# Kernel tuning notes

Hardware: AMD Instinct MI355X
Metric: run time of the kernel (lower is better)

Reference implementation:

```python
import jax, jax.numpy as jnp
import numpy as np

N, E, H, C = 50000, 800000, 4, 32   # nodes, edges, heads, per-head channels
EMB = 64                              # embedding_dim
VOCAB = 1000                          # input_dim (label vocab)


def _gat_layer(x, src, dst, W, a_src, a_dst, b):
    """PyG GATConv (concat heads, negative_slope=0.2, self-loops already in src/dst)."""
    n = x.shape[0]
    h = (x @ W).reshape(n, H, -1)                 # [N,H,C]
    al_s = (h * a_src).sum(-1)                    # [N,H]
    al_d = (h * a_dst).sum(-1)                    # [N,H]
    e = jax.nn.leaky_relu(al_s[src] + al_d[dst], 0.2)   # [E',H]
    m = jax.ops.segment_max(e, dst, num_segments=n)     # segment softmax (stable)
    p = jnp.exp(e - m[dst])
    s = jax.ops.segment_sum(p, dst, num_segments=n)
    alpha = p / (s[dst] + 1e-16)                  # [E',H]
    out = jax.ops.segment_sum(h[src] * alpha[..., None], dst, num_segments=n)
    return out.reshape(n, -1) + b                 # [N,H*C]


def setup_inputs() -> dict:
    key = jax.random.key(0)
    ks = jax.random.split(key, 16)
    def w(k, shape):
        return jax.random.normal(k, shape, jnp.float32) * 0.1
    return dict(
        label=jax.random.randint(ks[0], (N,), 0, VOCAB),
        edge_index=jax.random.randint(ks[1], (2, E), 0, N),
        weight=jax.random.uniform(ks[2], (E,), jnp.float32),
        request_quantity=jax.random.uniform(ks[3], (N,), jnp.float32),
        emb_table=w(ks[4], (VOCAB, EMB)),
        req_W=w(ks[5], (1, EMB)),
        req_b=jnp.zeros((EMB,), jnp.float32),
        W0=w(ks[6], (2 * EMB, H * C)), a_src0=w(ks[7], (H, C)), a_dst0=w(ks[8], (H, C)), b0=jnp.zeros((H * C,), jnp.float32),
        W1=w(ks[9], (H * C, H * C)), a_src1=w(ks[10], (H, C)), a_dst1=w(ks[11], (H, C)), b1=jnp.zeros((H * C,), jnp.float32),
        W2=w(ks[12], (H * C, H * C)), a_src2=w(ks[13], (H, C)), a_dst2=w(ks[14], (H, C)), b2=jnp.zeros((H * C,), jnp.float32),
    )


def reference(label, edge_index, weight, request_quantity, emb_table, req_W, req_b,
              W0, a_src0, a_dst0, b0, W1, a_src1, a_dst1, b1, W2, a_src2, a_dst2, b2):
    del weight  # GATConv(edge_dim=None): edge weights are not used in attention
    x_emb = emb_table[label]                                  # [N,EMB]
    rq = request_quantity
    rq = (rq - rq.mean()) / (rq.std(ddof=1) + 1e-6)           # torch std uses ddof=1
    req = rq[:, None] @ req_W + req_b                         # [N,EMB]
    x = jnp.concatenate([x_emb, req], axis=-1)                # [N,2*EMB]
    # PyG GATConv adds self-loops by default
    loops = jnp.arange(N)
    src = jnp.concatenate([edge_index[0], loops])
    dst = jnp.concatenate([edge_index[1], loops])
    gelu = lambda t: jax.nn.gelu(t, approximate=False)        # torch nn.GELU is exact
    x = gelu(_gat_layer(x, src, dst, W0, a_src0, a_dst0, b0))
    x = gelu(_gat_layer(x, src, dst, W1, a_src1, a_dst1, b1))
    x = gelu(_gat_layer(x, src, dst, W2, a_src2, a_dst2, b2))
    return x
```

## Files before the change

### kernel.cpp

```cpp
#include <hip/hip_runtime.h>
#include <hip/hip_fp16.h>
#include <math.h>

#define NN 50000
#define NE 800000
#define HC 128
#define NHEAD 4
#define EMB 64
#define STATS_BLOCKS 64
#define NB 196
#define HIST_BLOCKS 196
#define WPREP_BLOCKS 192
#define WT_ROW 136

typedef _Float16 f16x8 __attribute__((ext_vector_type(8)));
typedef float f32x4 __attribute__((ext_vector_type(4)));

__device__ __forceinline__ float lrelu(float x) { return x > 0.0f ? x : 0.2f * x; }
__device__ __forceinline__ float gelu_f(float x) {
    return 0.5f * x * (1.0f + erff(x * 0.70710678118654752440f));
}
__device__ __forceinline__ float sel4(float4 v, int h) {
    float r = v.x;
    r = (h == 1) ? v.y : r;
    r = (h == 2) ? v.z : r;
    r = (h == 3) ? v.w : r;
    return r;
}
__device__ __forceinline__ f16x8 cvt8(float4 a, float4 b) {
    f16x8 v;
    v[0] = (_Float16)a.x; v[1] = (_Float16)a.y; v[2] = (_Float16)a.z; v[3] = (_Float16)a.w;
    v[4] = (_Float16)b.x; v[5] = (_Float16)b.y; v[6] = (_Float16)b.z; v[7] = (_Float16)b.w;
    return v;
}

__global__ void prep_kernel(const float* __restrict__ rq, float* __restrict__ stats,
                            const int* __restrict__ dst, int* __restrict__ bucketCnt,
                            const float* __restrict__ W0, const float* __restrict__ W1,
                            const float* __restrict__ W2, _Float16* __restrict__ wt) {
    __shared__ float ls[4], ls2[4];
    __shared__ int cnt[NB];
    if (blockIdx.x < STATS_BLOCKS) {
        int i = blockIdx.x * 256 + threadIdx.x;
        float s = 0.f, s2 = 0.f;
        for (; i < NN; i += STATS_BLOCKS * 256) {
            float v = rq[i];
            s += v; s2 += v * v;
        }
        #pragma unroll
        for (int off = 32; off > 0; off >>= 1) {
            s  += __shfl_down(s, off);
            s2 += __shfl_down(s2, off);
        }
        int lane = threadIdx.x & 63, wid = threadIdx.x >> 6;
        if (lane == 0) { ls[wid] = s; ls2[wid] = s2; }
        __syncthreads();
        if (threadIdx.x == 0) {
            atomicAdd(&stats[0], ls[0] + ls[1] + ls[2] + ls[3]);
            atomicAdd(&stats[1], ls2[0] + ls2[1] + ls2[2] + ls2[3]);
        }
    } else if (blockIdx.x < STATS_BLOCKS + HIST_BLOCKS) {
        int bb = blockIdx.x - STATS_BLOCKS;
        for (int i = threadIdx.x; i < NB; i += 256) cnt[i] = 0;
        __syncthreads();
        int base = bb * 4096;
        #pragma unroll
        for (int it = 0; it < 16; it++) {
            int i = base + it * 256 + threadIdx.x;
            if (i < NE) atomicAdd(&cnt[dst[i] >> 8], 1);
        }
        __syncthreads();
        for (int i = threadIdx.x; i < NB; i += 256)
            if (cnt[i]) atomicAdd(&bucketCnt[i], cnt[i]);
    } else {
        int bb = blockIdx.x - STATS_BLOCKS - HIST_BLOCKS;
        int l = bb >> 6, blk = bb & 63;
        const float* W = (l == 0) ? W0 : (l == 1) ? W1 : W2;
        int idx = blk * 256 + threadIdx.x;
        int n = idx >> 7, k = idx & 127;
        wt[(size_t)l * 128 * WT_ROW + n * WT_ROW + k] = (_Float16)W[k * 128 + n];
    }
}

__device__ __forceinline__ void scan_buckets(const int* __restrict__ bucketCnt,
                                             int* sIncl ) {
    int t = threadIdx.x;
    int v = (t < NB) ? bucketCnt[t] : 0;
    sIncl[t] = v;
    __syncthreads();
    #pragma unroll
    for (int off = 1; off < 256; off <<= 1) {
        int add = (t >= off) ? sIncl[t - off] : 0;
        __syncthreads();
        sIncl[t] += add;
        __syncthreads();
    }
}

__global__ void binA_kernel(const int* __restrict__ src, const int* __restrict__ dst,
                            const int* __restrict__ bucketCnt, int* __restrict__ gcur,
                            int2* __restrict__ edge_tmp) {
    __shared__ int sIncl[256];
    __shared__ int sBaseE[256];
    __shared__ int cnt[NB];
    __shared__ int cur[NB];
    int t = threadIdx.x;
    scan_buckets(bucketCnt, sIncl);
    {
        int v = (t < NB) ? bucketCnt[t] : 0;
        sBaseE[t] = sIncl[t] - v;
    }
    for (int i = t; i < NB; i += 256) cnt[i] = 0;
    __syncthreads();
    int base = blockIdx.x * 4096;
    int d[16], s[16];
    #pragma unroll
    for (int it = 0; it < 16; it++) {
        int i = base + it * 256 + t;
        bool ok = i < NE;
        d[it] = ok ? dst[i] : -1;
        s[it] = ok ? src[i] : 0;
        if (ok) atomicAdd(&cnt[d[it] >> 8], 1);
    }
    __syncthreads();
    for (int i = t; i < NB; i += 256)
        cur[i] = cnt[i] ? (sBaseE[i] + atomicAdd(&gcur[i], cnt[i])) : 0;
    __syncthreads();
    #pragma unroll
    for (int it = 0; it < 16; it++) {
        if (d[it] >= 0) {
            int b = d[it] >> 8;
            int pos = atomicAdd(&cur[b], 1);
            edge_tmp[pos] = make_int2(s[it], d[it] & 255);
        }
    }
}

__global__ void binB_kernel(const int2* __restrict__ edge_tmp, const int* __restrict__ bucketCnt,
                            int* __restrict__ row_start, int* __restrict__ src_sorted) {
    __shared__ int sIncl[256];
    __shared__ int ldeg[256];
    __shared__ int lexcl[256];
    __shared__ int lcur[256];
    __shared__ int s_base, s_end;
    int b = blockIdx.x, t = threadIdx.x;
    scan_buckets(bucketCnt, sIncl);
    if (t == 0) {
        s_end = sIncl[b];
        s_base = sIncl[b] - bucketCnt[b];
    }
    ldeg[t] = 0;
    __syncthreads();
    int base = s_base, endb = s_end;
    for (int i = base + t; i < endb; i += 256)
        atomicAdd(&ldeg[edge_tmp[i].y], 1);
    __syncthreads();
    int v = ldeg[t];
    lexcl[t] = v;
    __syncthreads();
    #pragma unroll
    for (int off = 1; off < 256; off <<= 1) {
        int add = (t >= off) ? lexcl[t - off] : 0;
        __syncthreads();
        lexcl[t] += add;
        __syncthreads();
    }
    int excl = lexcl[t] - v;
    int node = b * 256 + t;
    if (node <= NN) row_start[node] = base + excl;
    lcur[t] = excl;
    __syncthreads();
    for (int i = base + t; i < endb; i += 256) {
        int2 e = edge_tmp[i];
        int pos = atomicAdd(&lcur[e.y], 1);
        src_sorted[base + pos] = e.x;
    }
}

template <int L0>
__launch_bounds__(256)
__global__ void gemm_al_kernel(const __half* __restrict__ xh, const _Float16* __restrict__ wt,
                               const float* __restrict__ a_src, const float* __restrict__ a_dst,
                               __half* __restrict__ h, float* __restrict__ als,
                               float* __restrict__ ald,
                               const int* __restrict__ label, const float* __restrict__ rq,
                               const float* __restrict__ emb, const float* __restrict__ reqW,
                               const float* __restrict__ reqb, const float* __restrict__ stats) {
    extern __shared__ char smem[];
    _Float16* sWt = (_Float16*)smem;
    _Float16* sX  = sWt + 128 * WT_ROW;
    int t = threadIdx.x;
    int w = t >> 6, l = t & 63;
    int col = l & 15, quad = l >> 4;
    int row0 = blockIdx.x * 64;

    {
        const f16x8* g = (const f16x8*)wt;
        f16x8* s = (f16x8*)sWt;
        #pragma unroll
        for (int i = 0; i < 9; i++) {
            int idx = t + 256 * i;
            if (idx < 128 * WT_ROW / 8) s[idx] = g[idx];
        }
    }
    if (L0) {
        float sum = stats[0], sumsq = stats[1];
        float mean = sum / (float)NN;
        float var = (sumsq - sum * sum / (float)NN) / (float)(NN - 1);
        float inv = 1.0f / (sqrtf(var) + 1e-6f);
        #pragma unroll
        for (int i = 0; i < 4; i++) {
            int idx = t + 256 * i;
            int r = idx >> 4;
            int q = idx & 15;
            int rr = row0 + r;
            f16x8 v;
            #pragma unroll
            for (int j = 0; j < 8; j++) v[j] = (_Float16)0.f;
            if (rr < NN) {
                if (q < 8) {
                    const float4* er = (const float4*)(emb + (size_t)label[rr] * EMB);
                    v = cvt8(er[q * 2], er[q * 2 + 1]);
                } else {
                    int j4 = (q - 8) * 2;
                    float4 w0 = ((const float4*)reqW)[j4],     b0 = ((const float4*)reqb)[j4];
                    float4 w1 = ((const float4*)reqW)[j4 + 1], b1 = ((const float4*)reqb)[j4 + 1];
                    float r2 = (rq[rr] - mean) * inv;
                    v = cvt8(make_float4(r2 * w0.x + b0.x, r2 * w0.y + b0.y,
                                         r2 * w0.z + b0.z, r2 * w0.w + b0.w),
                             make_float4(r2 * w1.x + b1.x, r2 * w1.y + b1.y,
                                         r2 * w1.z + b1.z, r2 * w1.w + b1.w));
                }
            }
            *(f16x8*)&sX[r * WT_ROW + q * 8] = v;
        }
    }
    __syncthreads();

    f16x8 afr[4];
    if (L0) {
        #pragma unroll
        for (int ks = 0; ks < 4; ks++)
            afr[ks] = *(const f16x8*)&sX[(w * 16 + col) * WT_ROW + ks * 32 + quad * 8];
    } else {
        int rr = row0 + w * 16 + col;
        const __half* xp = xh + (size_t)rr * 128;
        #pragma unroll
        for (int ks = 0; ks < 4; ks++)
            afr[ks] = *(const f16x8*)(xp + ks * 32 + quad * 8);
    }

    f32x4 zero = {0.f, 0.f, 0.f, 0.f};
    f32x4 acc[8];
    #pragma unroll
    for (int nt = 0; nt < 8; nt++) acc[nt] = zero;
    #pragma unroll
    for (int nt = 0; nt < 8; nt++) {
        #pragma unroll
        for (int ks = 0; ks < 4; ks++) {
            f16x8 bfr = *(const f16x8*)&sWt[(nt * 16 + col) * WT_ROW + ks * 32 + quad * 8];
            acc[nt] = __builtin_amdgcn_mfma_f32_16x16x32_f16(afr[ks], bfr, acc[nt], 0, 0, 0);
        }
    }
    __syncthreads();

    _Float16* sOut = sWt;
    #pragma unroll
    for (int nt = 0; nt < 8; nt++)
        #pragma unroll
        for (int r = 0; r < 4; r++)
            sOut[(w * 16 + quad * 4 + r) * WT_ROW + nt * 16 + col] = (_Float16)acc[nt][r];
    __builtin_amdgcn_wave_barrier();
    #pragma unroll
    for (int i = 0; i < 4; i++) {
        int u = l + 64 * i;
        int r = u >> 4, off = (u & 15) * 8;
        int rr = row0 + w * 16 + r;
        f16x8 v = *(const f16x8*)&sOut[(w * 16 + r) * WT_ROW + off];
        if (rr < NN) *(f16x8*)(h + (size_t)rr * 128 + off) = v;
    }

    float as[8], ad[8];
    #pragma unroll
    for (int nt = 0; nt < 8; nt++) {
        as[nt] = a_src[nt * 16 + col];
        ad[nt] = a_dst[nt * 16 + col];
    }
    #pragma unroll
    for (int r = 0; r < 4; r++) {
        float ps[4], pd[4];
        #pragma unroll
        for (int hd = 0; hd < 4; hd++) {
            ps[hd] = acc[2 * hd][r] * as[2 * hd] + acc[2 * hd + 1][r] * as[2 * hd + 1];
            pd[hd] = acc[2 * hd][r] * ad[2 * hd] + acc[2 * hd + 1][r] * ad[2 * hd + 1];
            ps[hd] += __shfl_xor(ps[hd], 1); pd[hd] += __shfl_xor(pd[hd], 1);
            ps[hd] += __shfl_xor(ps[hd], 2); pd[hd] += __shfl_xor(pd[hd], 2);
            ps[hd] += __shfl_xor(ps[hd], 4); pd[hd] += __shfl_xor(pd[hd], 4);
            ps[hd] += __shfl_xor(ps[hd], 8); pd[hd] += __shfl_xor(pd[hd], 8);
        }
        int rr = row0 + w * 16 + quad * 4 + r;
        if (col == 0 && rr < NN) {
            *(float4*)(als + (size_t)rr * 4) = make_float4(ps[0], ps[1], ps[2], ps[3]);
            *(float4*)(ald + (size_t)rr * 4) = make_float4(pd[0], pd[1], pd[2], pd[3]);
        }
    }
}

template <int FINAL>
__launch_bounds__(256)
__global__ void agg_kernel(const __half* __restrict__ h, const float* __restrict__ als_,
                           const float* __restrict__ ald_, const int* __restrict__ row_start,
                           const int* __restrict__ src_sorted, const float* __restrict__ bias,
                           float* __restrict__ outf, __half* __restrict__ outh) {
    __shared__ int2 lds_sp[4][4][130];
    int wid  = threadIdx.x >> 6;
    int lane = threadIdx.x & 63;
    int g    = lane >> 4;
    int cg   = lane & 15;
    int c0   = cg * 8;
    int head = cg >> 2;

    int nb = blockIdx.x * 16 + wid * 4;
    if (nb >= NN) return;
    int node = nb + g;

    int rs = row_start[node];
    int re = row_start[node + 1];
    int start = __shfl(rs, 0);
    int end   = __shfl(re, 48);
    int b1 = __shfl(rs, 16), b2 = __shfl(rs, 32), b3 = __shfl(rs, 48);

    float4 adv = *(const float4*)(ald_ + (size_t)node * 4);
    float4 avs = *(const float4*)(als_ + (size_t)node * 4);

    float p_self = __expf(lrelu(sel4(avs, head) + sel4(adv, head)));
    float s_sum = p_self;
    float acc[8];
    {
        f16x8 hv = *(const f16x8*)(h + (size_t)node * 128 + c0);
        #pragma unroll
        for (int j = 0; j < 8; j++) acc[j] = (float)hv[j] * p_self;
    }

    for (int base = start; base < end; base += 128) {
        int j0 = base + lane, j1 = base + 64 + lane;
        bool v0 = j0 < end, v1 = j1 < end;
        int my0 = v0 ? src_sorted[j0] : 0;
        int my1 = v1 ? src_sorted[j1] : 0;
        float4 av0 = *(const float4*)(als_ + (size_t)my0 * 4);
        float4 av1 = *(const float4*)(als_ + (size_t)my1 * 4);
        int o0 = (j0 >= b1) + (j0 >= b2) + (j0 >= b3);
        int o1 = (j1 >= b1) + (j1 >= b2) + (j1 >= b3);
        float4 d0 = *(const float4*)(ald_ + (size_t)(nb + (o0 > 3 ? 3 : o0)) * 4);
        float4 d1 = *(const float4*)(ald_ + (size_t)(nb + (o1 > 3 ? 3 : o1)) * 4);
        lds_sp[wid][0][lane] = make_int2(my0, __float_as_int(__expf(lrelu(av0.x + d0.x))));
        lds_sp[wid][1][lane] = make_int2(my0, __float_as_int(__expf(lrelu(av0.y + d0.y))));
        lds_sp[wid][2][lane] = make_int2(my0, __float_as_int(__expf(lrelu(av0.z + d0.z))));
        lds_sp[wid][3][lane] = make_int2(my0, __float_as_int(__expf(lrelu(av0.w + d0.w))));
        lds_sp[wid][0][64 + lane] = make_int2(my1, __float_as_int(__expf(lrelu(av1.x + d1.x))));
        lds_sp[wid][1][64 + lane] = make_int2(my1, __float_as_int(__expf(lrelu(av1.y + d1.y))));
        lds_sp[wid][2][64 + lane] = make_int2(my1, __float_as_int(__expf(lrelu(av1.z + d1.z))));
        lds_sp[wid][3][64 + lane] = make_int2(my1, __float_as_int(__expf(lrelu(av1.w + d1.w))));
        __builtin_amdgcn_wave_barrier();

        int lo  = rs > base ? rs : base;
        int hiw = base + 128;
        int hi  = re < hiw ? re : hiw;
        for (int k = lo; k < hi; k += 16) {
            float p[16];
            const __half* ap[16];
            #pragma unroll
            for (int i = 0; i < 16; i++) {
                int e = k + i;
                bool val = e < hi;
                int ec = (val ? e : hi - 1) - base;
                int2 sp = lds_sp[wid][head][ec];
                p[i] = val ? __int_as_float(sp.y) : 0.f;
                ap[i] = h + (size_t)sp.x * 128 + c0;
            }
            f16x8 raw[16];
            #pragma unroll
            for (int i = 0; i < 16; i++)
                raw[i] = *(const f16x8*)ap[i];
            #pragma unroll
            for (int i = 0; i < 16; i++) {
                s_sum += p[i];
                #pragma unroll
                for (int jj = 0; jj < 8; jj++)
                    acc[jj] += (float)raw[i][jj] * p[i];
            }
        }
        __builtin_amdgcn_wave_barrier();
    }

    float invs = 1.0f / (s_sum + 1e-16f);
    float4 bv0 = *(const float4*)(bias + c0);
    float4 bv1 = *(const float4*)(bias + c0 + 4);
    float ob[8] = {bv0.x, bv0.y, bv0.z, bv0.w, bv1.x, bv1.y, bv1.z, bv1.w};
    float o8[8];
    #pragma unroll
    for (int jj = 0; jj < 8; jj++) o8[jj] = gelu_f(acc[jj] * invs + ob[jj]);
    if (FINAL) {
        float* op = outf + (size_t)node * 128 + c0;
        *(float4*)op       = make_float4(o8[0], o8[1], o8[2], o8[3]);
        *(float4*)(op + 4) = make_float4(o8[4], o8[5], o8[6], o8[7]);
    } else {
        f16x8 hv;
        #pragma unroll
        for (int jj = 0; jj < 8; jj++) hv[jj] = (_Float16)o8[jj];
        *(f16x8*)(outh + (size_t)node * 128 + c0) = hv;
    }
}

extern "C" void kernel_launch(void* const* d_in, const int* in_sizes, int n_in,
                              void* d_out, int out_size, void* d_ws, size_t ws_size,
                              hipStream_t stream) {
    const int*   label = (const int*)d_in[0];
    const int*   eidx  = (const int*)d_in[1];
    const float* rq    = (const float*)d_in[3];
    const float* emb   = (const float*)d_in[4];
    const float* reqW  = (const float*)d_in[5];
    const float* reqb  = (const float*)d_in[6];
    const float* W[3]    = {(const float*)d_in[7],  (const float*)d_in[11], (const float*)d_in[15]};
    const float* asrc[3] = {(const float*)d_in[8],  (const float*)d_in[12], (const float*)d_in[16]};
    const float* adst[3] = {(const float*)d_in[9],  (const float*)d_in[13], (const float*)d_in[17]};
    const float* bias[3] = {(const float*)d_in[10], (const float*)d_in[14], (const float*)d_in[18]};

    const int* e_src = eidx;
    const int* e_dst = eidx + NE;

    char* ws = (char*)d_ws;
    size_t off = 0;
    auto A = [&](size_t n) { size_t o = off; off += (n + 255) & ~(size_t)255; return o; };
    size_t o_bcnt  = A(256 * 4);
    size_t o_gcur  = A(256 * 4);
    size_t o_stats = A(8);
    size_t zero_bytes = off;
    size_t o_row   = A((size_t)(NN + 1) * 4);
    size_t o_etmp  = A((size_t)NE * 8);
    size_t o_srcS  = A((size_t)NE * 4);
    size_t o_wt    = A((size_t)3 * 128 * WT_ROW * 2);
    size_t o_x     = A((size_t)NN * 128 * 2);
    size_t o_h     = A((size_t)NN * 128 * 2);
    size_t o_als   = A((size_t)NN * 4 * 4);
    size_t o_ald   = A((size_t)NN * 4 * 4);
    (void)ws_size; (void)n_in; (void)in_sizes; (void)out_size;

    int*      bcnt  = (int*)(ws + o_bcnt);
    int*      gcur  = (int*)(ws + o_gcur);
    float*    stats = (float*)(ws + o_stats);
    int*      rowst = (int*)(ws + o_row);
    int2*     etmp  = (int2*)(ws + o_etmp);
    int*      srcS  = (int*)(ws + o_srcS);
    _Float16* wt    = (_Float16*)(ws + o_wt);
    __half*   xh    = (__half*)(ws + o_x);
    __half*   h     = (__half*)(ws + o_h);
    float*    als   = (float*)(ws + o_als);
    float*    ald   = (float*)(ws + o_ald);

    (void)hipMemsetAsync(ws, 0, zero_bytes, stream);

    prep_kernel<<<STATS_BLOCKS + HIST_BLOCKS + WPREP_BLOCKS, 256, 0, stream>>>(
        rq, stats, e_dst, bcnt, W[0], W[1], W[2], wt);
    binA_kernel<<<HIST_BLOCKS, 256, 0, stream>>>(e_src, e_dst, bcnt, gcur, etmp);
    binB_kernel<<<NB, 256, 0, stream>>>(etmp, bcnt, rowst, srcS);

    const int gemm_blocks = (NN + 63) / 64;
    const int agg_blocks = (NN + 15) / 16;
    const int smem_l0 = (128 + 64) * WT_ROW * 2;
    const int smem_ln = 128 * WT_ROW * 2;
    for (int l = 0; l < 3; l++) {
        const _Float16* wtl = wt + (size_t)l * 128 * WT_ROW;
        if (l == 0)
            gemm_al_kernel<1><<<gemm_blocks, 256, smem_l0, stream>>>(
                xh, wtl, asrc[l], adst[l], h, als, ald, label, rq, emb, reqW, reqb, stats);
        else
            gemm_al_kernel<0><<<gemm_blocks, 256, smem_ln, stream>>>(
                xh, wtl, asrc[l], adst[l], h, als, ald, label, rq, emb, reqW, reqb, stats);
        if (l == 2)
            agg_kernel<1><<<agg_blocks, 256, 0, stream>>>(h, als, ald, rowst, srcS, bias[l],
                                                          (float*)d_out, nullptr);
        else
            agg_kernel<0><<<agg_blocks, 256, 0, stream>>>(h, als, ald, rowst, srcS, bias[l],
                                                          nullptr, xh);
    }
}
```

Measured before the change: 293.6 us.

## Fuse aggregation with next-layer GEMM and replace two-pass binning with degree-based CSR scatter

Result: slower. 371.3 us (+26.5%).

```diff
diff --git a/kernel.cpp b/kernel.cpp
--- a/kernel.cpp
+++ b/kernel.cpp
@@ -5,13 +5,14 @@
 #define NN 50000
 #define NE 800000
 #define HC 128
-#define NHEAD 4
 #define EMB 64
 #define STATS_BLOCKS 64
 #define NB 196
 #define HIST_BLOCKS 196
 #define WPREP_BLOCKS 192
 #define WT_ROW 136
+#define GEMM_BLOCKS 782
+#define SCAT_BLOCKS 782
 
 typedef _Float16 f16x8 __attribute__((ext_vector_type(8)));
 typedef float f32x4 __attribute__((ext_vector_type(4)));
@@ -36,6 +37,7 @@
 
 __global__ void prep_kernel(const float* __restrict__ rq, float* __restrict__ stats,
                             const int* __restrict__ dst, int* __restrict__ bucketCnt,
+                            int* __restrict__ degree,
                             const float* __restrict__ W0, const float* __restrict__ W1,
                             const float* __restrict__ W2, _Float16* __restrict__ wt) {
     __shared__ float ls[4], ls2[4];
@@ -67,7 +69,11 @@
         #pragma unroll
         for (int it = 0; it < 16; it++) {
             int i = base + it * 256 + threadIdx.x;
-            if (i < NE) atomicAdd(&cnt[dst[i] >> 8], 1);
+            if (i < NE) {
+                int d = dst[i];
+                atomicAdd(&degree[d], 1);
+                atomicAdd(&cnt[d >> 8], 1);
+            }
         }
         __syncthreads();
         for (int i = threadIdx.x; i < NB; i += 256)
@@ -97,65 +103,15 @@
     }
 }
 
-__global__ void binA_kernel(const int* __restrict__ src, const int* __restrict__ dst,
-                            const int* __restrict__ bucketCnt, int* __restrict__ gcur,
-                            int2* __restrict__ edge_tmp) {
+__global__ void row_kernel(const int* __restrict__ bucketCnt, const int* __restrict__ degree,
+                           int* __restrict__ row_start, int* __restrict__ cursor) {
     __shared__ int sIncl[256];
-    __shared__ int sBaseE[256];
-    __shared__ int cnt[NB];
-    __shared__ int cur[NB];
-    int t = threadIdx.x;
-    scan_buckets(bucketCnt, sIncl);
-    {
-        int v = (t < NB) ? bucketCnt[t] : 0;
-        sBaseE[t] = sIncl[t] - v;
-    }
-    for (int i = t; i < NB; i += 256) cnt[i] = 0;
-    __syncthreads();
-    int base = blockIdx.x * 4096;
-    int d[16], s[16];
-    #pragma unroll
-    for (int it = 0; it < 16; it++) {
-        int i = base + it * 256 + t;
-        bool ok = i < NE;
-        d[it] = ok ? dst[i] : -1;
-        s[it] = ok ? src[i] : 0;
-        if (ok) atomicAdd(&cnt[d[it] >> 8], 1);
-    }
-    __syncthreads();
-    for (int i = t; i < NB; i += 256)
-        cur[i] = cnt[i] ? (sBaseE[i] + atomicAdd(&gcur[i], cnt[i])) : 0;
-    __syncthreads();
-    #pragma unroll
-    for (int it = 0; it < 16; it++) {
-        if (d[it] >= 0) {
-            int b = d[it] >> 8;
-            int pos = atomicAdd(&cur[b], 1);
-            edge_tmp[pos] = make_int2(s[it], d[it] & 255);
-        }
-    }
-}
-
-__global__ void binB_kernel(const int2* __restrict__ edge_tmp, const int* __restrict__ bucketCnt,
-                            int* __restrict__ row_start, int* __restrict__ src_sorted) {
-    __shared__ int sIncl[256];
-    __shared__ int ldeg[256];
     __shared__ int lexcl[256];
-    __shared__ int lcur[256];
-    __shared__ int s_base, s_end;
     int b = blockIdx.x, t = threadIdx.x;
     scan_buckets(bucketCnt, sIncl);
-    if (t == 0) {
-        s_end = sIncl[b];
-        s_base = sIncl[b] - bucketCnt[b];
-    }
-    ldeg[t] = 0;
-    __syncthreads();
-    int base = s_base, endb = s_end;
-    for (int i = base + t; i < endb; i += 256)
-        atomicAdd(&ldeg[edge_tmp[i].y], 1);
-    __syncthreads();
-    int v = ldeg[t];
+    int bucket_base = sIncl[b] - bucketCnt[b];
+    int node = b * 256 + t;
+    int v = (node < NN) ? degree[node] : 0;
     lexcl[t] = v;
     __syncthreads();
     #pragma unroll
@@ -166,32 +122,108 @@
         __syncthreads();
     }
     int excl = lexcl[t] - v;
-    int node = b * 256 + t;
-    if (node <= NN) row_start[node] = base + excl;
-    lcur[t] = excl;
+    if (node <= NN) row_start[node] = bucket_base + excl;
+    if (node < NN) cursor[node] = bucket_base + excl;
+}
+
+__device__ __forceinline__ void mfma_epilogue(_Float16* sWt, _Float16* sX,
+        const float* __restrict__ a_src, const float* __restrict__ a_dst,
+        __half* __restrict__ h, float* __restrict__ als, float* __restrict__ ald,
+        int row0) {
+    int t = threadIdx.x;
+    int w = t >> 6, l = t & 63;
+    int col = l & 15, quad = l >> 4;
+
+    f16x8 afr[4];
+    #pragma unroll
+    for (int ks = 0; ks < 4; ks++)
+        afr[ks] = *(const f16x8*)&sX[(w * 16 + col) * WT_ROW + ks * 32 + quad * 8];
+
+    f32x4 zero = {0.f, 0.f, 0.f, 0.f};
+    f32x4 acc[8];
+    #pragma unroll
+    for (int nt = 0; nt < 8; nt++) acc[nt] = zero;
+    #pragma unroll
+    for (int nt = 0; nt < 8; nt++) {
+        #pragma unroll
+        for (int ks = 0; ks < 4; ks++) {
+            f16x8 bfr = *(const f16x8*)&sWt[(nt * 16 + col) * WT_ROW + ks * 32 + quad * 8];
+            acc[nt] = __builtin_amdgcn_mfma_f32_16x16x32_f16(afr[ks], bfr, acc[nt], 0, 0, 0);
+        }
+    }
     __syncthreads();
-    for (int i = base + t; i < endb; i += 256) {
-        int2 e = edge_tmp[i];
-        int pos = atomicAdd(&lcur[e.y], 1);
-        src_sorted[base + pos] = e.x;
-    }
-}
-
-template <int L0>
+
+    _Float16* sOut = sWt;
+    #pragma unroll
+    for (int nt = 0; nt < 8; nt++)
+        #pragma unroll
+        for (int r = 0; r < 4; r++)
+            sOut[(w * 16 + quad * 4 + r) * WT_ROW + nt * 16 + col] = (_Float16)acc[nt][r];
+    __builtin_amdgcn_wave_barrier();
+    #pragma unroll
+    for (int i = 0; i < 4; i++) {
+        int u = l + 64 * i;
+        int r = u >> 4, off = (u & 15) * 8;
+        int rr = row0 + w * 16 + r;
+        f16x8 v = *(const f16x8*)&sOut[(w * 16 + r) * WT_ROW + off];
+        if (rr < NN) *(f16x8*)(h + (size_t)rr * 128 + off) = v;
+    }
+
+    float as[8], ad[8];
+    #pragma unroll
+    for (int nt = 0; nt < 8; nt++) {
+        as[nt] = a_src[nt * 16 + col];
+        ad[nt] = a_dst[nt * 16 + col];
+    }
+    #pragma unroll
+    for (int r = 0; r < 4; r++) {
+        float ps[4], pd[4];
+        #pragma unroll
+        for (int hd = 0; hd < 4; hd++) {
+            ps[hd] = acc[2 * hd][r] * as[2 * hd] + acc[2 * hd + 1][r] * as[2 * hd + 1];
+            pd[hd] = acc[2 * hd][r] * ad[2 * hd] + acc[2 * hd + 1][r] * ad[2 * hd + 1];
+            ps[hd] += __shfl_xor(ps[hd], 1); pd[hd] += __shfl_xor(pd[hd], 1);
+            ps[hd] += __shfl_xor(ps[hd], 2); pd[hd] += __shfl_xor(pd[hd], 2);
+            ps[hd] += __shfl_xor(ps[hd], 4); pd[hd] += __shfl_xor(pd[hd], 4);
+            ps[hd] += __shfl_xor(ps[hd], 8); pd[hd] += __shfl_xor(pd[hd], 8);
+        }
+        int rr = row0 + w * 16 + quad * 4 + r;
+        if (col == 0 && rr < NN) {
+            *(float4*)(als + (size_t)rr * 4) = make_float4(ps[0], ps[1], ps[2], ps[3]);
+            *(float4*)(ald + (size_t)rr * 4) = make_float4(pd[0], pd[1], pd[2], pd[3]);
+        }
+    }
+}
+
 __launch_bounds__(256)
-__global__ void gemm_al_kernel(const __half* __restrict__ xh, const _Float16* __restrict__ wt,
-                               const float* __restrict__ a_src, const float* __restrict__ a_dst,
-                               __half* __restrict__ h, float* __restrict__ als,
-                               float* __restrict__ ald,
-                               const int* __restrict__ label, const float* __restrict__ rq,
-                               const float* __restrict__ emb, const float* __restrict__ reqW,
-                               const float* __restrict__ reqb, const float* __restrict__ stats) {
+__global__ void gemm0_scatter_kernel(const _Float16* __restrict__ wt,
+                                     const float* __restrict__ a_src, const float* __restrict__ a_dst,
+                                     __half* __restrict__ h, float* __restrict__ als,
+                                     float* __restrict__ ald,
+                                     const int* __restrict__ label, const float* __restrict__ rq,
+                                     const float* __restrict__ emb, const float* __restrict__ reqW,
+                                     const float* __restrict__ reqb, const float* __restrict__ stats,
+                                     const int* __restrict__ src, const int* __restrict__ dst,
+                                     int* __restrict__ cursor, int* __restrict__ src_sorted) {
     extern __shared__ char smem[];
+    if (blockIdx.x >= GEMM_BLOCKS) {
+        int sb = blockIdx.x - GEMM_BLOCKS;
+        int base = sb * 1024;
+        #pragma unroll
+        for (int it = 0; it < 4; it++) {
+            int i = base + it * 256 + threadIdx.x;
+            if (i < NE) {
+                int d = dst[i];
+                int s = src[i];
+                int pos = atomicAdd(&cursor[d], 1);
+                src_sorted[pos] = s;
+            }
+        }
+        return;
+    }
     _Float16* sWt = (_Float16*)smem;
     _Float16* sX  = sWt + 128 * WT_ROW;
     int t = threadIdx.x;
-    int w = t >> 6, l = t & 63;
-    int col = l & 15, quad = l >> 4;
     int row0 = blockIdx.x * 64;
 
     {
@@ -203,7 +235,7 @@
             if (idx < 128 * WT_ROW / 8) s[idx] = g[idx];
         }
     }
-    if (L0) {
+    {
         float sum = stats[0], sumsq = stats[1];
         float mean = sum / (float)NN;
         float var = (sumsq - sum * sum / (float)NN) / (float)(NN - 1);
@@ -236,82 +268,123 @@
         }
     }
     __syncthreads();
-
-    f16x8 afr[4];
-    if (L0) {
-        #pragma unroll
-        for (int ks = 0; ks < 4; ks++)
-            afr[ks] = *(const f16x8*)&sX[(w * 16 + col) * WT_ROW + ks * 32 + quad * 8];
-    } else {
-        int rr = row0 + w * 16 + col;
-        const __half* xp = xh + (size_t)rr * 128;
-        #pragma unroll
-        for (int ks = 0; ks < 4; ks++)
-            afr[ks] = *(const f16x8*)(xp + ks * 32 + quad * 8);
-    }
-
-    f32x4 zero = {0.f, 0.f, 0.f, 0.f};
-    f32x4 acc[8];
-    #pragma unroll
-    for (int nt = 0; nt < 8; nt++) acc[nt] = zero;
-    #pragma unroll
-    for (int nt = 0; nt < 8; nt++) {
-        #pragma unroll
-        for (int ks = 0; ks < 4; ks++) {
-            f16x8 bfr = *(const f16x8*)&sWt[(nt * 16 + col) * WT_ROW + ks * 32 + quad * 8];
-            acc[nt] = __builtin_amdgcn_mfma_f32_16x16x32_f16(afr[ks], bfr, acc[nt], 0, 0, 0);
+    mfma_epilogue(sWt, sX, a_src, a_dst, h, als, ald, row0);
+}
+
+__launch_bounds__(256)
+__global__ void layer_kernel(const __half* __restrict__ hp, const float* __restrict__ alsp,
+                             const float* __restrict__ aldp, const int* __restrict__ row_start,
+                             const int* __restrict__ src_sorted, const float* __restrict__ biasp,
+                             const _Float16* __restrict__ wt,
+                             const float* __restrict__ a_src, const float* __restrict__ a_dst,
+                             __half* __restrict__ ho, float* __restrict__ also_,
+                             float* __restrict__ aldo) {
+    extern __shared__ char smem[];
+    _Float16* sWt = (_Float16*)smem;
+    _Float16* sX  = sWt + 128 * WT_ROW;
+    int t = threadIdx.x;
+    int w = t >> 6, lane = t & 63;
+    int g = lane >> 4;
+    int cg = lane & 15;
+    int c0 = cg * 8;
+    int head = cg >> 2;
+    int row0 = blockIdx.x * 64;
+
+    {
+        const f16x8* gp = (const f16x8*)wt;
+        f16x8* s = (f16x8*)sWt;
+        #pragma unroll
+        for (int i = 0; i < 9; i++) {
+            int idx = t + 256 * i;
+            if (idx < 128 * WT_ROW / 8) s[idx] = gp[idx];
+        }
+    }
+
+    for (int round = 0; round < 4; round++) {
+        int nb = row0 + (w << 4) + (round << 2);
+        if (nb < NN) {
+            int node = nb + g;
+            int rs = row_start[node], re = row_start[node + 1];
+            int start = __shfl(rs, 0), end = __shfl(re, 48);
+            int b1 = __shfl(rs, 16), b2 = __shfl(rs, 32), b3 = __shfl(rs, 48);
+
+            float4 adv = *(const float4*)(aldp + (size_t)node * 4);
+            float4 avs = *(const float4*)(alsp + (size_t)node * 4);
+            float p_self = __expf(lrelu(sel4(avs, head) + sel4(adv, head)));
+            float s_sum = p_self;
+            float acc[8];
+            {
+                f16x8 hv = *(const f16x8*)(hp + (size_t)node * 128 + c0);
+                #pragma unroll
+                for (int j = 0; j < 8; j++) acc[j] = (float)hv[j] * p_self;
+            }
+
+            for (int base = start; base < end; base += 64) {
+                int j = base + lane;
+                bool v = j < end;
+                int my = v ? src_sorted[j] : 0;
+                float4 av = *(const float4*)(alsp + (size_t)my * 4);
+                int o = (j >= b1) + (j >= b2) + (j >= b3);
+                float4 dv = *(const float4*)(aldp + (size_t)(nb + (o > 3 ? 3 : o)) * 4);
+                float px = __expf(lrelu(av.x + dv.x));
+                float py = __expf(lrelu(av.y + dv.y));
+                float pz = __expf(lrelu(av.z + dv.z));
+                float pw = __expf(lrelu(av.w + dv.w));
+
+                int lo = rs > base ? rs : base;
+                int hiw = base + 64;
+                int hi = re < hiw ? re : hiw;
+                for (int kk = 0; kk < 64; kk += 8) {
+                    int e0 = lo + kk;
+                    if (!__any(e0 < hi)) break;
+                    float p[8]; int sxi[8];
+                    #pragma unroll
+                    for (int i = 0; i < 8; i++) {
+                        int e = e0 + i;
+                        bool val = e < hi;
+                        int ec = (val ? e : hi - 1) - base;
+                        ec = ec < 0 ? 0 : ec;
+                        int s_ = __shfl(my, ec);
+                        float qx = __shfl(px, ec), qy = __shfl(py, ec);
+                        float qz = __shfl(pz, ec), qw = __shfl(pw, ec);
+                        float pv = sel4(make_float4(qx, qy, qz, qw), head);
+                        p[i] = val ? pv : 0.f;
+                        sxi[i] = s_;
+                    }
+                    f16x8 raw[8];
+                    #pragma unroll
+                    for (int i = 0; i < 8; i++)
+                        raw[i] = *(const f16x8*)(hp + (size_t)sxi[i] * 128 + c0);
+                    #pragma unroll
+                    for (int i = 0; i < 8; i++) {
+                        s_sum += p[i];
+                        #pragma unroll
+                        for (int jj = 0; jj < 8; jj++)
+                            acc[jj] += (float)raw[i][jj] * p[i];
+                    }
+                }
+            }
+
+            float invs = 1.0f / (s_sum + 1e-16f);
+            float4 bv0 = *(const float4*)(biasp + c0);
+            float4 bv1 = *(const float4*)(biasp + c0 + 4);
+            float ob[8] = {bv0.x, bv0.y, bv0.z, bv0.w, bv1.x, bv1.y, bv1.z, bv1.w};
+            f16x8 o;
+            #pragma unroll
+            for (int jj = 0; jj < 8; jj++)
+                o[jj] = (_Float16)gelu_f(acc[jj] * invs + ob[jj]);
+            *(f16x8*)&sX[(nb - row0 + g) * WT_ROW + c0] = o;
         }
     }
     __syncthreads();
-
-    _Float16* sOut = sWt;
-    #pragma unroll
-    for (int nt = 0; nt < 8; nt++)
-        #pragma unroll
-        for (int r = 0; r < 4; r++)
-            sOut[(w * 16 + quad * 4 + r) * WT_ROW + nt * 16 + col] = (_Float16)acc[nt][r];
-    __builtin_amdgcn_wave_barrier();
-    #pragma unroll
-    for (int i = 0; i < 4; i++) {
-        int u = l + 64 * i;
-        int r = u >> 4, off = (u & 15) * 8;
-        int rr = row0 + w * 16 + r;
-        f16x8 v = *(const f16x8*)&sOut[(w * 16 + r) * WT_ROW + off];
-        if (rr < NN) *(f16x8*)(h + (size_t)rr * 128 + off) = v;
-    }
-
-    float as[8], ad[8];
-    #pragma unroll
-    for (int nt = 0; nt < 8; nt++) {
-        as[nt] = a_src[nt * 16 + col];
-        ad[nt] = a_dst[nt * 16 + col];
-    }
-    #pragma unroll
-    for (int r = 0; r < 4; r++) {
-        float ps[4], pd[4];
-        #pragma unroll
-        for (int hd = 0; hd < 4; hd++) {
-            ps[hd] = acc[2 * hd][r] * as[2 * hd] + acc[2 * hd + 1][r] * as[2 * hd + 1];
-            pd[hd] = acc[2 * hd][r] * ad[2 * hd] + acc[2 * hd + 1][r] * ad[2 * hd + 1];
-            ps[hd] += __shfl_xor(ps[hd], 1); pd[hd] += __shfl_xor(pd[hd], 1);
-            ps[hd] += __shfl_xor(ps[hd], 2); pd[hd] += __shfl_xor(pd[hd], 2);
-            ps[hd] += __shfl_xor(ps[hd], 4); pd[hd] += __shfl_xor(pd[hd], 4);
-            ps[hd] += __shfl_xor(ps[hd], 8); pd[hd] += __shfl_xor(pd[hd], 8);
-        }
-        int rr = row0 + w * 16 + quad * 4 + r;
-        if (col == 0 && rr < NN) {
-            *(float4*)(als + (size_t)rr * 4) = make_float4(ps[0], ps[1], ps[2], ps[3]);
-            *(float4*)(ald + (size_t)rr * 4) = make_float4(pd[0], pd[1], pd[2], pd[3]);
-        }
-    }
-}
-
-template <int FINAL>
+    mfma_epilogue(sWt, sX, a_src, a_dst, ho, also_, aldo, row0);
+}
+
 __launch_bounds__(256)
-__global__ void agg_kernel(const __half* __restrict__ h, const float* __restrict__ als_,
-                           const float* __restrict__ ald_, const int* __restrict__ row_start,
-                           const int* __restrict__ src_sorted, const float* __restrict__ bias,
-                           float* __restrict__ outf, __half* __restrict__ outh) {
+__global__ void agg_final_kernel(const __half* __restrict__ h, const float* __restrict__ als_,
+                                 const float* __restrict__ ald_, const int* __restrict__ row_start,
+                                 const int* __restrict__ src_sorted, const float* __restrict__ bias,
+                                 float* __restrict__ outf) {
     __shared__ int2 lds_sp[4][4][130];
     int wid  = threadIdx.x >> 6;
     int lane = threadIdx.x & 63;
@@ -400,16 +473,9 @@
     float o8[8];
     #pragma unroll
     for (int jj = 0; jj < 8; jj++) o8[jj] = gelu_f(acc[jj] * invs + ob[jj]);
-    if (FINAL) {
-        float* op = outf + (size_t)node * 128 + c0;
-        *(float4*)op       = make_float4(o8[0], o8[1], o8[2], o8[3]);
-        *(float4*)(op + 4) = make_float4(o8[4], o8[5], o8[6], o8[7]);
-    } else {
-        f16x8 hv;
-        #pragma unroll
-        for (int jj = 0; jj < 8; jj++) hv[jj] = (_Float16)o8[jj];
-        *(f16x8*)(outh + (size_t)node * 128 + c0) = hv;
-    }
+    float* op = outf + (size_t)node * 128 + c0;
+    *(float4*)op       = make_float4(o8[0], o8[1], o8[2], o8[3]);
+    *(float4*)(op + 4) = make_float4(o8[4], o8[5], o8[6], o8[7]);
 }
 
 extern "C" void kernel_launch(void* const* d_in, const int* in_sizes, int n_in,
@@ -433,55 +499,51 @@
     size_t off = 0;
     auto A = [&](size_t n) { size_t o = off; off += (n + 255) & ~(size_t)255; return o; };
     size_t o_bcnt  = A(256 * 4);
-    size_t o_gcur  = A(256 * 4);
     size_t o_stats = A(8);
+    size_t o_deg   = A((size_t)NN * 4);
     size_t zero_bytes = off;
     size_t o_row   = A((size_t)(NN + 1) * 4);
-    size_t o_etmp  = A((size_t)NE * 8);
+    size_t o_cur   = A((size_t)NN * 4);
     size_t o_srcS  = A((size_t)NE * 4);
     size_t o_wt    = A((size_t)3 * 128 * WT_ROW * 2);
-    size_t o_x     = A((size_t)NN * 128 * 2);
-    size_t o_h     = A((size_t)NN * 128 * 2);
-    size_t o_als   = A((size_t)NN * 4 * 4);
-    size_t o_ald   = A((size_t)NN * 4 * 4);
+    size_t o_h0    = A((size_t)NN * 128 * 2);
+    size_t o_h1    = A((size_t)NN * 128 * 2);
+    size_t o_als0  = A((size_t)NN * 4 * 4);
+    size_t o_ald0  = A((size_t)NN * 4 * 4);
+    size_t o_als1  = A((size_t)NN * 4 * 4);
+    size_t o_ald1  = A((size_t)NN * 4 * 4);
     (void)ws_size; (void)n_in; (void)in_sizes; (void)out_size;
 
     int*      bcnt  = (int*)(ws + o_bcnt);
-    int*      gcur  = (int*)(ws + o_gcur);
     float*    stats = (float*)(ws + o_stats);
+    int*      deg   = (int*)(ws + o_deg);
     int*      rowst = (int*)(ws + o_row);
-    int2*     etmp  = (int2*)(ws + o_etmp);
+    int*      cur   = (int*)(ws + o_cur);
     int*      srcS  = (int*)(ws + o_srcS);
     _Float16* wt    = (_Float16*)(ws + o_wt);
-    __half*   xh    = (__half*)(ws + o_x);
-    __half*   h     = (__half*)(ws + o_h);
-    float*    als   = (float*)(ws + o_als);
-    float*    ald   = (float*)(ws + o_ald);
+    __half*   h0    = (__half*)(ws + o_h0);
+    __half*   h1    = (__half*)(ws + o_h1);
+    float*    als0  = (float*)(ws + o_als0);
+    float*    ald0  = (float*)(ws + o_ald0);
+    float*    als1  = (float*)(ws + o_als1);
+    float*    ald1  = (float*)(ws + o_ald1);
 
     (void)hipMemsetAsync(ws, 0, zero_bytes, stream);
 
+    const int smem = (128 + 64) * WT_ROW * 2;
+
     prep_kernel<<<STATS_BLOCKS + HIST_BLOCKS + WPREP_BLOCKS, 256, 0, stream>>>(
-        rq, stats, e_dst, bcnt, W[0], W[1], W[2], wt);
-    binA_kernel<<<HIST_BLOCKS, 256, 0, stream>>>(e_src, e_dst, bcnt, gcur, etmp);
-    binB_kernel<<<NB, 256, 0, stream>>>(etmp, bcnt, rowst, srcS);
-
-    const int gemm_blocks = (NN + 63) / 64;
-    const int agg_blocks = (NN + 15) / 16;
-    const int smem_l0 = (128 + 64) * WT_ROW * 2;
-    const int smem_ln = 128 * WT_ROW * 2;
-    for (int l = 0; l < 3; l++) {
-        const _Float16* wtl = wt + (size_t)l * 128 * WT_ROW;
-        if (l == 0)
-            gemm_al_kernel<1><<<gemm_blocks, 256, smem_l0, stream>>>(
-                xh, wtl, asrc[l], adst[l], h, als, ald, label, rq, emb, reqW, reqb, stats);
-        else
-            gemm_al_kernel<0><<<gemm_blocks, 256, smem_ln, stream>>>(
-                xh, wtl, asrc[l], adst[l], h, als, ald, label, rq, emb, reqW, reqb, stats);
-        if (l == 2)
-            agg_kernel<1><<<agg_blocks, 256, 0, stream>>>(h, als, ald, rowst, srcS, bias[l],
-                                                          (float*)d_out, nullptr);
-        else
-            agg_kernel<0><<<agg_blocks, 256, 0, stream>>>(h, als, ald, rowst, srcS, bias[l],
-                                                          nullptr, xh);
-    }
-}
+        rq, stats, e_dst, bcnt, deg, W[0], W[1], W[2], wt);
+    row_kernel<<<NB, 256, 0, stream>>>(bcnt, deg, rowst, cur);
+    gemm0_scatter_kernel<<<GEMM_BLOCKS + SCAT_BLOCKS, 256, smem, stream>>>(
+        wt, asrc[0], adst[0], h0, als0, ald0, label, rq, emb, reqW, reqb, stats,
+        e_src, e_dst, cur, srcS);
+    layer_kernel<<<GEMM_BLOCKS, 256, smem, stream>>>(
+        h0, als0, ald0, rowst, srcS, bias[0],
+        wt + (size_t)1 * 128 * WT_ROW, asrc[1], adst[1], h1, als1, ald1);
+    layer_kernel<<<GEMM_BLOCKS, 256, smem, stream>>>(
+        h1, als1, ald1, rowst, srcS, bias[1],
+        wt + (size_t)2 * 128 * WT_ROW, asrc[2], adst[2], h0, als0, ald0);
+    agg_final_kernel<<<(NN + 15) / 16, 256, 0, stream>>>(
+        h0, als0, ald0, rowst, srcS, bias[2], (float*)d_out);
+}
```
